# Optimization experiments

Measured on AMD Instinct MI355X. Metric: run time of the kernel, lower is better.

Reference implementation:

```python
import jax, jax.numpy as jnp
import numpy as np

E = 64          # num_experts
DIM = 1024      # model dim
HID = 512       # per-expert FFN hidden dim
N = 65536       # total routed tokens (1024 per expert)


def setup_inputs() -> dict:
    key = jax.random.key(0)
    k_x, k1, k2, k3 = jax.random.split(key, 4)
    x = jax.random.normal(k_x, (N, DIM), dtype=jnp.float32)
    # learned params: w1/w3 [E, HID, DIM], w2 [E, DIM, HID] (trunc_normal std 0.02 ~ normal*0.02)
    w1 = jax.random.normal(k1, (E, HID, DIM), dtype=jnp.float32) * 0.02
    w2 = jax.random.normal(k2, (E, DIM, HID), dtype=jnp.float32) * 0.02
    w3 = jax.random.normal(k3, (E, HID, DIM), dtype=jnp.float32) * 0.02
    num_tokens_per_expert = jnp.full((E,), N // E, dtype=jnp.int32)
    return {"x": x, "w1": w1, "w2": w2, "w3": w3,
            "num_tokens_per_expert": num_tokens_per_expert}


def reference(x, w1, w2, w3, num_tokens_per_expert):
    # Grouped-GEMM SwiGLU expert FFN (torch._grouped_mm path, bf16 compute).
    bf16 = jnp.bfloat16
    xb = x.astype(bf16)                                   # [N, DIM]
    g = num_tokens_per_expert                             # [E] int32 group sizes
    w1t = jnp.swapaxes(w1.astype(bf16), 1, 2)             # [E, DIM, HID]
    w3t = jnp.swapaxes(w3.astype(bf16), 1, 2)             # [E, DIM, HID]
    w2t = jnp.swapaxes(w2.astype(bf16), 1, 2)             # [E, HID, DIM]
    h = jax.nn.silu(jax.lax.ragged_dot(xb, w1t, g))       # [N, HID]
    h = h * jax.lax.ragged_dot(xb, w3t, g)                # fused gate
    out = jax.lax.ragged_dot(h, w2t, g)                   # [N, DIM]
    return out.astype(x.dtype)
```

## Files before the change

### kernel.cpp

```cpp
#include <hip/hip_runtime.h>
#include <hip/hip_bf16.h>
#include <stdint.h>

#define NE   64
#define DIM  1024
#define HID  512
#define TPE  1024

typedef __attribute__((ext_vector_type(8)))  __bf16          bf16x8;
typedef __attribute__((ext_vector_type(16))) float           f32x16;
typedef __attribute__((ext_vector_type(8)))  unsigned short  ushort8_t;
typedef __attribute__((ext_vector_type(4)))  float           float4_t;

__device__ __forceinline__ unsigned short f2bf(float f) {
  return __builtin_bit_cast(unsigned short, static_cast<__bf16>(f));
}
__device__ __forceinline__ float bf2f(unsigned short u) {
  unsigned int x = ((unsigned int)u) << 16;
  return __builtin_bit_cast(float, x);
}
__device__ __forceinline__ ushort8_t pack8(float4_t a, float4_t b) {
  ushort8_t r;
  r[0] = f2bf(a[0]); r[1] = f2bf(a[1]); r[2] = f2bf(a[2]); r[3] = f2bf(a[3]);
  r[4] = f2bf(b[0]); r[5] = f2bf(b[1]); r[6] = f2bf(b[2]); r[7] = f2bf(b[3]);
  return r;
}
__device__ __forceinline__ bf16x8 ldsfrag(const unsigned short* p) {
  return __builtin_bit_cast(bf16x8, *reinterpret_cast<const ushort8_t*>(p));
}

__device__ __forceinline__ void barrier_lgkm() {
  asm volatile("s_waitcnt lgkmcnt(0)" ::: "memory");
  __builtin_amdgcn_s_barrier();
}

#define LDK 40

__device__ __forceinline__ int xcd_swizzle(int bid, int nwg) {
  return (bid & 7) * (nwg >> 3) + (bid >> 3);
}

#define P1_NKT (DIM / 32)

__global__ __launch_bounds__(256, 3) void p1_kernel(
    const float* __restrict__ X, const float* __restrict__ W1,
    const float* __restrict__ W3, unsigned short* __restrict__ H) {
  __shared__ __align__(16) unsigned short lA [2][128 * LDK];
  __shared__ __align__(16) unsigned short lB1[2][ 64 * LDK];
  __shared__ __align__(16) unsigned short lB3[2][ 64 * LDK];

  const int tile = xcd_swizzle(blockIdx.x, NE * 8 * 8);
  const int e  = tile >> 6;
  const int tn = (tile >> 3) & 7;
  const int tm = tile & 7;
  const int t  = threadIdx.x;

  const float* gA  = X  + (size_t)(e * TPE + tm * 128) * DIM;
  const float* gB1 = W1 + ((size_t)e * HID + tn * 64) * DIM;
  const float* gB3 = W3 + ((size_t)e * HID + tn * 64) * DIM;

  const int ar = t >> 2, ac = (t & 3) * 8;

  float4_t a0[2][2], b10[2], b30[2];
  float4_t a1[2][2], b11[2], b31[2];

  auto load_g = [&](float4_t (&a)[2][2], float4_t (&b1)[2], float4_t (&b3)[2],
                    int kt) {
#pragma unroll
    for (int i = 0; i < 2; ++i) {
      const size_t o = (size_t)(ar + 64 * i) * DIM + kt * 32 + ac;
      a[i][0] = *reinterpret_cast<const float4_t*>(gA + o);
      a[i][1] = *reinterpret_cast<const float4_t*>(gA + o + 4);
    }
    const size_t ob = (size_t)ar * DIM + kt * 32 + ac;
    b1[0] = *reinterpret_cast<const float4_t*>(gB1 + ob);
    b1[1] = *reinterpret_cast<const float4_t*>(gB1 + ob + 4);
    b3[0] = *reinterpret_cast<const float4_t*>(gB3 + ob);
    b3[1] = *reinterpret_cast<const float4_t*>(gB3 + ob + 4);
  };
  auto store_l = [&](int buf, float4_t (&a)[2][2], float4_t (&b1)[2],
                     float4_t (&b3)[2]) {
#pragma unroll
    for (int i = 0; i < 2; ++i)
      *reinterpret_cast<ushort8_t*>(&lA[buf][(ar + 64 * i) * LDK + ac]) =
          pack8(a[i][0], a[i][1]);
    *reinterpret_cast<ushort8_t*>(&lB1[buf][ar * LDK + ac]) = pack8(b1[0], b1[1]);
    *reinterpret_cast<ushort8_t*>(&lB3[buf][ar * LDK + ac]) = pack8(b3[0], b3[1]);
  };

  const int lane = t & 63;
  const int wv   = t >> 6;
  const int wr   = wv >> 1, wc = wv & 1;
  const int lr   = lane & 31;
  const int ks   = (lane >> 5) * 8;

  f32x16 acc1[2], acc3[2];
#pragma unroll
  for (int m = 0; m < 2; ++m)
#pragma unroll
    for (int i = 0; i < 16; ++i) { acc1[m][i] = 0.f; acc3[m][i] = 0.f; }

  auto mfma_phase = [&](int buf) {
#pragma unroll
    for (int kk = 0; kk < 2; ++kk) {
      bf16x8 am[2];
#pragma unroll
      for (int m = 0; m < 2; ++m)
        am[m] = ldsfrag(&lA[buf][(wr * 64 + m * 32 + lr) * LDK + kk * 16 + ks]);
      const bf16x8 b1 = ldsfrag(&lB1[buf][(wc * 32 + lr) * LDK + kk * 16 + ks]);
      const bf16x8 b3 = ldsfrag(&lB3[buf][(wc * 32 + lr) * LDK + kk * 16 + ks]);
#pragma unroll
      for (int m = 0; m < 2; ++m) {
        acc1[m] = __builtin_amdgcn_mfma_f32_32x32x16_bf16(am[m], b1, acc1[m], 0, 0, 0);
        acc3[m] = __builtin_amdgcn_mfma_f32_32x32x16_bf16(am[m], b3, acc3[m], 0, 0, 0);
      }
    }
  };

  load_g(a0, b10, b30, 0);
  load_g(a1, b11, b31, 1);
  for (int kt = 0; kt < P1_NKT; kt += 2) {
    store_l(0, a0, b10, b30);
    if (kt + 2 < P1_NKT) load_g(a0, b10, b30, kt + 2);
    barrier_lgkm();
    mfma_phase(0);
    store_l(1, a1, b11, b31);
    if (kt + 3 < P1_NKT) load_g(a1, b11, b31, kt + 3);
    barrier_lgkm();
    mfma_phase(1);
  }

  const int tokBase = e * TPE + tm * 128 + wr * 64;
  const int hid     = tn * 64 + wc * 32 + lr;
  const int ks4     = (lane >> 5) * 4;
#pragma unroll
  for (int m = 0; m < 2; ++m)
#pragma unroll
    for (int r = 0; r < 16; ++r) {
      const int rr  = (r & 3) + 8 * (r >> 2) + ks4;
      const int tok = tokBase + m * 32 + rr;
      const float av = bf2f(f2bf(acc1[m][r]));
      const float bv = bf2f(f2bf(acc3[m][r]));
      const float s  = av / (1.0f + __expf(-av));
      H[(size_t)tok * HID + hid] = f2bf(s * bv);
    }
}

#define P2_NKT (HID / 32)

__global__ __launch_bounds__(256, 3) void p2_kernel(
    const unsigned short* __restrict__ Hin, const float* __restrict__ W2,
    float* __restrict__ OUT) {
  __shared__ __align__(16) unsigned short lA[2][128 * LDK];
  __shared__ __align__(16) unsigned short lB[2][128 * LDK];

  const int tile = xcd_swizzle(blockIdx.x, NE * 8 * 8);
  const int e  = tile >> 6;
  const int tn = (tile >> 3) & 7;
  const int tm = tile & 7;
  const int t  = threadIdx.x;

  const unsigned short* gA = Hin + (size_t)(e * TPE + tm * 128) * HID;
  const float*          gB = W2  + ((size_t)e * DIM + tn * 128) * HID;

  const int arow = t >> 1, acol = (t & 1) * 16;
  const int br = t >> 2, bc = (t & 3) * 8;

  ushort8_t ha0[2], ha1[2];
  float4_t  wb0[2][2], wb1[2][2];

  auto load_g = [&](ushort8_t (&ha)[2], float4_t (&wb)[2][2], int kt) {
    const size_t ao = (size_t)arow * HID + kt * 32 + acol;
    ha[0] = *reinterpret_cast<const ushort8_t*>(gA + ao);
    ha[1] = *reinterpret_cast<const ushort8_t*>(gA + ao + 8);
#pragma unroll
    for (int i = 0; i < 2; ++i) {
      const size_t bo = (size_t)(br + 64 * i) * HID + kt * 32 + bc;
      wb[i][0] = *reinterpret_cast<const float4_t*>(gB + bo);
      wb[i][1] = *reinterpret_cast<const float4_t*>(gB + bo + 4);
    }
  };
  auto store_l = [&](int buf, ushort8_t (&ha)[2], float4_t (&wb)[2][2]) {
    const int ai = arow * LDK + acol;
    *reinterpret_cast<ushort8_t*>(&lA[buf][ai])     = ha[0];
    *reinterpret_cast<ushort8_t*>(&lA[buf][ai + 8]) = ha[1];
#pragma unroll
    for (int i = 0; i < 2; ++i)
      *reinterpret_cast<ushort8_t*>(&lB[buf][(br + 64 * i) * LDK + bc]) =
          pack8(wb[i][0], wb[i][1]);
  };

  const int lane = t & 63;
  const int wv   = t >> 6;
  const int wr   = wv >> 1, wc = wv & 1;
  const int lr   = lane & 31;
  const int ks   = (lane >> 5) * 8;

  f32x16 acc[2][2];
#pragma unroll
  for (int m = 0; m < 2; ++m)
#pragma unroll
    for (int n = 0; n < 2; ++n)
#pragma unroll
      for (int i = 0; i < 16; ++i) acc[m][n][i] = 0.f;

  auto mfma_phase = [&](int buf) {
#pragma unroll
    for (int kk = 0; kk < 2; ++kk) {
      bf16x8 am[2], bn[2];
#pragma unroll
      for (int m = 0; m < 2; ++m)
        am[m] = ldsfrag(&lA[buf][(wr * 64 + m * 32 + lr) * LDK + kk * 16 + ks]);
#pragma unroll
      for (int n = 0; n < 2; ++n)
        bn[n] = ldsfrag(&lB[buf][(wc * 64 + n * 32 + lr) * LDK + kk * 16 + ks]);
#pragma unroll
      for (int m = 0; m < 2; ++m)
#pragma unroll
        for (int n = 0; n < 2; ++n)
          acc[m][n] = __builtin_amdgcn_mfma_f32_32x32x16_bf16(am[m], bn[n], acc[m][n], 0, 0, 0);
    }
  };

  load_g(ha0, wb0, 0);
  load_g(ha1, wb1, 1);
  for (int kt = 0; kt < P2_NKT; kt += 2) {
    store_l(0, ha0, wb0);
    if (kt + 2 < P2_NKT) load_g(ha0, wb0, kt + 2);
    barrier_lgkm();
    mfma_phase(0);

    store_l(1, ha1, wb1);
    if (kt + 3 < P2_NKT) load_g(ha1, wb1, kt + 3);
    barrier_lgkm();
    mfma_phase(1);
  }

  const int tokBase = e * TPE + tm * 128 + wr * 64;
  const int dBase   = tn * 128 + wc * 64;
  const int ks4     = (lane >> 5) * 4;
#pragma unroll
  for (int m = 0; m < 2; ++m)
#pragma unroll
    for (int n = 0; n < 2; ++n)
#pragma unroll
      for (int r = 0; r < 16; ++r) {
        const int rr  = (r & 3) + 8 * (r >> 2) + ks4;
        const int tok = tokBase + m * 32 + rr;
        const int d   = dBase + n * 32 + lr;
        OUT[(size_t)tok * DIM + d] = bf2f(f2bf(acc[m][n][r]));
      }
}

extern "C" void kernel_launch(void* const* d_in, const int* in_sizes, int n_in,
                              void* d_out, int out_size, void* d_ws, size_t ws_size,
                              hipStream_t stream) {
  (void)in_sizes; (void)n_in; (void)out_size; (void)ws_size;
  const float* X  = (const float*)d_in[0];
  const float* W1 = (const float*)d_in[1];
  const float* W2 = (const float*)d_in[2];
  const float* W3 = (const float*)d_in[3];

  unsigned short* H = (unsigned short*)d_ws;
  float* OUT = (float*)d_out;

  p1_kernel<<<dim3(NE * 8 * 8), dim3(256), 0, stream>>>(X, W1, W3, H);
  p2_kernel<<<dim3(NE * 8 * 8), dim3(256), 0, stream>>>(H, W2, OUT);
}
```

Measured before the change: 520.3 us.

## Double M tile to 256 rows and switch to 16x16x32 MFMA fragments

Both kernels now give each block 256 tokens instead of 128, which halves the grid. Each weight tile is reused across twice as many rows, so fewer fp32 weight bytes are reloaded per token. The MFMA instruction changes from 32x32x16 to 16x16x32, with more accumulators per wave (8x2 for the gate pair, 8x4 for the down projection). The cost is much higher register pressure, lowered occupancy bounds (3 to 2), larger LDS use, and fewer blocks to cover the CUs.

```diff
diff --git a/kernel.cpp b/kernel.cpp
--- a/kernel.cpp
+++ b/kernel.cpp
@@ -8,7 +8,7 @@
 #define TPE  1024
 
 typedef __attribute__((ext_vector_type(8)))  __bf16          bf16x8;
-typedef __attribute__((ext_vector_type(16))) float           f32x16;
+typedef __attribute__((ext_vector_type(4)))  float           f32x4;
 typedef __attribute__((ext_vector_type(8)))  unsigned short  ushort8_t;
 typedef __attribute__((ext_vector_type(4)))  float           float4_t;
 
@@ -42,32 +42,32 @@
 
 #define P1_NKT (DIM / 32)
 
-__global__ __launch_bounds__(256, 3) void p1_kernel(
+__global__ __launch_bounds__(256, 2) void p1_kernel(
     const float* __restrict__ X, const float* __restrict__ W1,
     const float* __restrict__ W3, unsigned short* __restrict__ H) {
-  __shared__ __align__(16) unsigned short lA [2][128 * LDK];
+  __shared__ __align__(16) unsigned short lA [2][256 * LDK];
   __shared__ __align__(16) unsigned short lB1[2][ 64 * LDK];
   __shared__ __align__(16) unsigned short lB3[2][ 64 * LDK];
 
-  const int tile = xcd_swizzle(blockIdx.x, NE * 8 * 8);
-  const int e  = tile >> 6;
-  const int tn = (tile >> 3) & 7;
-  const int tm = tile & 7;
+  const int tile = xcd_swizzle(blockIdx.x, NE * 4 * 8);
+  const int e  = tile >> 5;
+  const int tn = (tile >> 2) & 7;
+  const int tm = tile & 3;
   const int t  = threadIdx.x;
 
-  const float* gA  = X  + (size_t)(e * TPE + tm * 128) * DIM;
+  const float* gA  = X  + (size_t)(e * TPE + tm * 256) * DIM;
   const float* gB1 = W1 + ((size_t)e * HID + tn * 64) * DIM;
   const float* gB3 = W3 + ((size_t)e * HID + tn * 64) * DIM;
 
   const int ar = t >> 2, ac = (t & 3) * 8;
 
-  float4_t a0[2][2], b10[2], b30[2];
-  float4_t a1[2][2], b11[2], b31[2];
-
-  auto load_g = [&](float4_t (&a)[2][2], float4_t (&b1)[2], float4_t (&b3)[2],
+  float4_t a0[4][2], b10[2], b30[2];
+  float4_t a1[4][2], b11[2], b31[2];
+
+  auto load_g = [&](float4_t (&a)[4][2], float4_t (&b1)[2], float4_t (&b3)[2],
                     int kt) {
 #pragma unroll
-    for (int i = 0; i < 2; ++i) {
+    for (int i = 0; i < 4; ++i) {
       const size_t o = (size_t)(ar + 64 * i) * DIM + kt * 32 + ac;
       a[i][0] = *reinterpret_cast<const float4_t*>(gA + o);
       a[i][1] = *reinterpret_cast<const float4_t*>(gA + o + 4);
@@ -78,10 +78,10 @@
     b3[0] = *reinterpret_cast<const float4_t*>(gB3 + ob);
     b3[1] = *reinterpret_cast<const float4_t*>(gB3 + ob + 4);
   };
-  auto store_l = [&](int buf, float4_t (&a)[2][2], float4_t (&b1)[2],
+  auto store_l = [&](int buf, float4_t (&a)[4][2], float4_t (&b1)[2],
                      float4_t (&b3)[2]) {
 #pragma unroll
-    for (int i = 0; i < 2; ++i)
+    for (int i = 0; i < 4; ++i)
       *reinterpret_cast<ushort8_t*>(&lA[buf][(ar + 64 * i) * LDK + ac]) =
           pack8(a[i][0], a[i][1]);
     *reinterpret_cast<ushort8_t*>(&lB1[buf][ar * LDK + ac]) = pack8(b1[0], b1[1]);
@@ -91,28 +91,32 @@
   const int lane = t & 63;
   const int wv   = t >> 6;
   const int wr   = wv >> 1, wc = wv & 1;
-  const int lr   = lane & 31;
-  const int ks   = (lane >> 5) * 8;
-
-  f32x16 acc1[2], acc3[2];
-#pragma unroll
-  for (int m = 0; m < 2; ++m)
-#pragma unroll
-    for (int i = 0; i < 16; ++i) { acc1[m][i] = 0.f; acc3[m][i] = 0.f; }
+  const int fr   = lane & 15;
+  const int ks   = (lane >> 4) * 8;
+
+  f32x4 acc1[8][2], acc3[8][2];
+#pragma unroll
+  for (int m = 0; m < 8; ++m)
+#pragma unroll
+    for (int n = 0; n < 2; ++n)
+#pragma unroll
+      for (int i = 0; i < 4; ++i) { acc1[m][n][i] = 0.f; acc3[m][n][i] = 0.f; }
 
   auto mfma_phase = [&](int buf) {
-#pragma unroll
-    for (int kk = 0; kk < 2; ++kk) {
-      bf16x8 am[2];
-#pragma unroll
-      for (int m = 0; m < 2; ++m)
-        am[m] = ldsfrag(&lA[buf][(wr * 64 + m * 32 + lr) * LDK + kk * 16 + ks]);
-      const bf16x8 b1 = ldsfrag(&lB1[buf][(wc * 32 + lr) * LDK + kk * 16 + ks]);
-      const bf16x8 b3 = ldsfrag(&lB3[buf][(wc * 32 + lr) * LDK + kk * 16 + ks]);
-#pragma unroll
-      for (int m = 0; m < 2; ++m) {
-        acc1[m] = __builtin_amdgcn_mfma_f32_32x32x16_bf16(am[m], b1, acc1[m], 0, 0, 0);
-        acc3[m] = __builtin_amdgcn_mfma_f32_32x32x16_bf16(am[m], b3, acc3[m], 0, 0, 0);
+    bf16x8 b1f[2], b3f[2];
+#pragma unroll
+    for (int n = 0; n < 2; ++n) {
+      const int bi = (wc * 32 + n * 16 + fr) * LDK + ks;
+      b1f[n] = ldsfrag(&lB1[buf][bi]);
+      b3f[n] = ldsfrag(&lB3[buf][bi]);
+    }
+#pragma unroll
+    for (int m = 0; m < 8; ++m) {
+      const bf16x8 af = ldsfrag(&lA[buf][(wr * 128 + m * 16 + fr) * LDK + ks]);
+#pragma unroll
+      for (int n = 0; n < 2; ++n) {
+        acc1[m][n] = __builtin_amdgcn_mfma_f32_16x16x32_bf16(af, b1f[n], acc1[m][n], 0, 0, 0);
+        acc3[m][n] = __builtin_amdgcn_mfma_f32_16x16x32_bf16(af, b3f[n], acc3[m][n], 0, 0, 0);
       }
     }
   };
@@ -130,95 +134,92 @@
     mfma_phase(1);
   }
 
-  const int tokBase = e * TPE + tm * 128 + wr * 64;
-  const int hid     = tn * 64 + wc * 32 + lr;
-  const int ks4     = (lane >> 5) * 4;
-#pragma unroll
-  for (int m = 0; m < 2; ++m)
-#pragma unroll
-    for (int r = 0; r < 16; ++r) {
-      const int rr  = (r & 3) + 8 * (r >> 2) + ks4;
-      const int tok = tokBase + m * 32 + rr;
-      const float av = bf2f(f2bf(acc1[m][r]));
-      const float bv = bf2f(f2bf(acc3[m][r]));
-      const float s  = av / (1.0f + __expf(-av));
-      H[(size_t)tok * HID + hid] = f2bf(s * bv);
-    }
+  const int tokBase = e * TPE + tm * 256 + wr * 128 + (lane >> 4) * 4;
+  const int hidBase = tn * 64 + wc * 32;
+#pragma unroll
+  for (int m = 0; m < 8; ++m)
+#pragma unroll
+    for (int n = 0; n < 2; ++n)
+#pragma unroll
+      for (int r = 0; r < 4; ++r) {
+        const int tok = tokBase + m * 16 + r;
+        const int hid = hidBase + n * 16 + fr;
+        const float av = bf2f(f2bf(acc1[m][n][r]));
+        const float bv = bf2f(f2bf(acc3[m][n][r]));
+        const float s  = av / (1.0f + __expf(-av));
+        H[(size_t)tok * HID + hid] = f2bf(s * bv);
+      }
 }
 
 #define P2_NKT (HID / 32)
 
-__global__ __launch_bounds__(256, 3) void p2_kernel(
+__global__ __launch_bounds__(256, 2) void p2_kernel(
     const unsigned short* __restrict__ Hin, const float* __restrict__ W2,
     float* __restrict__ OUT) {
-  __shared__ __align__(16) unsigned short lA[2][128 * LDK];
+  __shared__ __align__(16) unsigned short lA[2][256 * LDK];
   __shared__ __align__(16) unsigned short lB[2][128 * LDK];
 
-  const int tile = xcd_swizzle(blockIdx.x, NE * 8 * 8);
-  const int e  = tile >> 6;
-  const int tn = (tile >> 3) & 7;
-  const int tm = tile & 7;
+  const int tile = xcd_swizzle(blockIdx.x, NE * 4 * 8);
+  const int e  = tile >> 5;
+  const int tn = (tile >> 2) & 7;
+  const int tm = tile & 3;
   const int t  = threadIdx.x;
 
-  const unsigned short* gA = Hin + (size_t)(e * TPE + tm * 128) * HID;
+  const unsigned short* gA = Hin + (size_t)(e * TPE + tm * 256) * HID;
   const float*          gB = W2  + ((size_t)e * DIM + tn * 128) * HID;
 
-  const int arow = t >> 1, acol = (t & 1) * 16;
-  const int br = t >> 2, bc = (t & 3) * 8;
-
-  ushort8_t ha0[2], ha1[2];
+  const int ar = t >> 2, ac = (t & 3) * 8;
+
+  ushort8_t ha0[4], ha1[4];
   float4_t  wb0[2][2], wb1[2][2];
 
-  auto load_g = [&](ushort8_t (&ha)[2], float4_t (&wb)[2][2], int kt) {
-    const size_t ao = (size_t)arow * HID + kt * 32 + acol;
-    ha[0] = *reinterpret_cast<const ushort8_t*>(gA + ao);
-    ha[1] = *reinterpret_cast<const ushort8_t*>(gA + ao + 8);
+  auto load_g = [&](ushort8_t (&ha)[4], float4_t (&wb)[2][2], int kt) {
+#pragma unroll
+    for (int i = 0; i < 4; ++i)
+      ha[i] = *reinterpret_cast<const ushort8_t*>(
+          gA + (size_t)(ar + 64 * i) * HID + kt * 32 + ac);
 #pragma unroll
     for (int i = 0; i < 2; ++i) {
-      const size_t bo = (size_t)(br + 64 * i) * HID + kt * 32 + bc;
+      const size_t bo = (size_t)(ar + 64 * i) * HID + kt * 32 + ac;
       wb[i][0] = *reinterpret_cast<const float4_t*>(gB + bo);
       wb[i][1] = *reinterpret_cast<const float4_t*>(gB + bo + 4);
     }
   };
-  auto store_l = [&](int buf, ushort8_t (&ha)[2], float4_t (&wb)[2][2]) {
-    const int ai = arow * LDK + acol;
-    *reinterpret_cast<ushort8_t*>(&lA[buf][ai])     = ha[0];
-    *reinterpret_cast<ushort8_t*>(&lA[buf][ai + 8]) = ha[1];
+  auto store_l = [&](int buf, ushort8_t (&ha)[4], float4_t (&wb)[2][2]) {
+#pragma unroll
+    for (int i = 0; i < 4; ++i)
+      *reinterpret_cast<ushort8_t*>(&lA[buf][(ar + 64 * i) * LDK + ac]) = ha[i];
 #pragma unroll
     for (int i = 0; i < 2; ++i)
-      *reinterpret_cast<ushort8_t*>(&lB[buf][(br + 64 * i) * LDK + bc]) =
+      *reinterpret_cast<ushort8_t*>(&lB[buf][(ar + 64 * i) * LDK + ac]) =
           pack8(wb[i][0], wb[i][1]);
   };
 
   const int lane = t & 63;
   const int wv   = t >> 6;
   const int wr   = wv >> 1, wc = wv & 1;
-  const int lr   = lane & 31;
-  const int ks   = (lane >> 5) * 8;
-
-  f32x16 acc[2][2];
-#pragma unroll
-  for (int m = 0; m < 2; ++m)
-#pragma unroll
-    for (int n = 0; n < 2; ++n)
-#pragma unroll
-      for (int i = 0; i < 16; ++i) acc[m][n][i] = 0.f;
+  const int fr   = lane & 15;
+  const int ks   = (lane >> 4) * 8;
+
+  f32x4 acc[8][4];
+#pragma unroll
+  for (int m = 0; m < 8; ++m)
+#pragma unroll
+    for (int n = 0; n < 4; ++n)
+#pragma unroll
+      for (int i = 0; i < 4; ++i) acc[m][n][i] = 0.f;
 
   auto mfma_phase = [&](int buf) {
-#pragma unroll
-    for (int kk = 0; kk < 2; ++kk) {
-      bf16x8 am[2], bn[2];
-#pragma unroll
-      for (int m = 0; m < 2; ++m)
-        am[m] = ldsfrag(&lA[buf][(wr * 64 + m * 32 + lr) * LDK + kk * 16 + ks]);
-#pragma unroll
-      for (int n = 0; n < 2; ++n)
-        bn[n] = ldsfrag(&lB[buf][(wc * 64 + n * 32 + lr) * LDK + kk * 16 + ks]);
-#pragma unroll
-      for (int m = 0; m < 2; ++m)
-#pragma unroll
-        for (int n = 0; n < 2; ++n)
-          acc[m][n] = __builtin_amdgcn_mfma_f32_32x32x16_bf16(am[m], bn[n], acc[m][n], 0, 0, 0);
+    bf16x8 bfr[4];
+#pragma unroll
+    for (int n = 0; n < 4; ++n)
+      bfr[n] = ldsfrag(&lB[buf][(wc * 64 + n * 16 + fr) * LDK + ks]);
+#pragma unroll
+    for (int m = 0; m < 8; ++m) {
+      const bf16x8 af = ldsfrag(&lA[buf][(wr * 128 + m * 16 + fr) * LDK + ks]);
+#pragma unroll
+      for (int n = 0; n < 4; ++n)
+        acc[m][n] = __builtin_amdgcn_mfma_f32_16x16x32_bf16(af, bfr[n], acc[m][n], 0, 0, 0);
     }
   };
 
@@ -229,25 +230,22 @@
     if (kt + 2 < P2_NKT) load_g(ha0, wb0, kt + 2);
     barrier_lgkm();
     mfma_phase(0);
-
     store_l(1, ha1, wb1);
     if (kt + 3 < P2_NKT) load_g(ha1, wb1, kt + 3);
     barrier_lgkm();
     mfma_phase(1);
   }
 
-  const int tokBase = e * TPE + tm * 128 + wr * 64;
+  const int tokBase = e * TPE + tm * 256 + wr * 128 + (lane >> 4) * 4;
   const int dBase   = tn * 128 + wc * 64;
-  const int ks4     = (lane >> 5) * 4;
-#pragma unroll
-  for (int m = 0; m < 2; ++m)
-#pragma unroll
-    for (int n = 0; n < 2; ++n)
-#pragma unroll
-      for (int r = 0; r < 16; ++r) {
-        const int rr  = (r & 3) + 8 * (r >> 2) + ks4;
-        const int tok = tokBase + m * 32 + rr;
-        const int d   = dBase + n * 32 + lr;
+#pragma unroll
+  for (int m = 0; m < 8; ++m)
+#pragma unroll
+    for (int n = 0; n < 4; ++n)
+#pragma unroll
+      for (int r = 0; r < 4; ++r) {
+        const int tok = tokBase + m * 16 + r;
+        const int d   = dBase + n * 16 + fr;
         OUT[(size_t)tok * DIM + d] = bf2f(f2bf(acc[m][n][r]));
       }
 }
@@ -264,6 +262,6 @@
   unsigned short* H = (unsigned short*)d_ws;
   float* OUT = (float*)d_out;
 
-  p1_kernel<<<dim3(NE * 8 * 8), dim3(256), 0, stream>>>(X, W1, W3, H);
-  p2_kernel<<<dim3(NE * 8 * 8), dim3(256), 0, stream>>>(H, W2, OUT);
-}
+  p1_kernel<<<dim3(NE * 4 * 8), dim3(256), 0, stream>>>(X, W1, W3, H);
+  p2_kernel<<<dim3(NE * 4 * 8), dim3(256), 0, stream>>>(H, W2, OUT);
+}
```

Result: no change. 517.5 us (-0.5%).

## Switch waves to 32-row x full-N tiling and single-buffer B prefetch

Applied to the files above, without the earlier changes.

Both kernels change the wave layout from a 2x2 wave grid to four waves, each owning 32 rows and the full N width of the block tile. W1 and W3 are merged into one LDS B buffer. The register prefetch of B drops from two sets to one, loaded one k-step ahead, while A keeps its two-deep prefetch. This lowers register pressure and changes the LDS fragment traffic: one A fragment and four B fragments per k-step instead of two and two. In exchange, B fragment LDS reads rise and B global loads get less latency hiding.

```diff
diff --git a/kernel.cpp b/kernel.cpp
--- a/kernel.cpp
+++ b/kernel.cpp
@@ -45,9 +45,8 @@
 __global__ __launch_bounds__(256, 3) void p1_kernel(
     const float* __restrict__ X, const float* __restrict__ W1,
     const float* __restrict__ W3, unsigned short* __restrict__ H) {
-  __shared__ __align__(16) unsigned short lA [2][128 * LDK];
-  __shared__ __align__(16) unsigned short lB1[2][ 64 * LDK];
-  __shared__ __align__(16) unsigned short lB3[2][ 64 * LDK];
+  __shared__ __align__(16) unsigned short lA[2][128 * LDK];
+  __shared__ __align__(16) unsigned short lB[2][128 * LDK];
 
   const int tile = xcd_swizzle(blockIdx.x, NE * 8 * 8);
   const int e  = tile >> 6;
@@ -56,91 +55,92 @@
   const int t  = threadIdx.x;
 
   const float* gA  = X  + (size_t)(e * TPE + tm * 128) * DIM;
-  const float* gB1 = W1 + ((size_t)e * HID + tn * 64) * DIM;
-  const float* gB3 = W3 + ((size_t)e * HID + tn * 64) * DIM;
+  const float* gW1 = W1 + ((size_t)e * HID + tn * 64) * DIM;
+  const float* gW3 = W3 + ((size_t)e * HID + tn * 64) * DIM;
 
   const int ar = t >> 2, ac = (t & 3) * 8;
 
-  float4_t a0[2][2], b10[2], b30[2];
-  float4_t a1[2][2], b11[2], b31[2];
-
-  auto load_g = [&](float4_t (&a)[2][2], float4_t (&b1)[2], float4_t (&b3)[2],
-                    int kt) {
+  float4_t a0[2][2], a1[2][2];
+  float4_t bb[2][2];
+
+  auto load_gA = [&](float4_t (&a)[2][2], int kt) {
 #pragma unroll
     for (int i = 0; i < 2; ++i) {
       const size_t o = (size_t)(ar + 64 * i) * DIM + kt * 32 + ac;
       a[i][0] = *reinterpret_cast<const float4_t*>(gA + o);
       a[i][1] = *reinterpret_cast<const float4_t*>(gA + o + 4);
     }
-    const size_t ob = (size_t)ar * DIM + kt * 32 + ac;
-    b1[0] = *reinterpret_cast<const float4_t*>(gB1 + ob);
-    b1[1] = *reinterpret_cast<const float4_t*>(gB1 + ob + 4);
-    b3[0] = *reinterpret_cast<const float4_t*>(gB3 + ob);
-    b3[1] = *reinterpret_cast<const float4_t*>(gB3 + ob + 4);
-  };
-  auto store_l = [&](int buf, float4_t (&a)[2][2], float4_t (&b1)[2],
-                     float4_t (&b3)[2]) {
+  };
+  auto load_gB = [&](int kt) {
+    const size_t o = (size_t)ar * DIM + kt * 32 + ac;
+    bb[0][0] = *reinterpret_cast<const float4_t*>(gW1 + o);
+    bb[0][1] = *reinterpret_cast<const float4_t*>(gW1 + o + 4);
+    bb[1][0] = *reinterpret_cast<const float4_t*>(gW3 + o);
+    bb[1][1] = *reinterpret_cast<const float4_t*>(gW3 + o + 4);
+  };
+  auto store_lA = [&](int buf, float4_t (&a)[2][2]) {
 #pragma unroll
     for (int i = 0; i < 2; ++i)
       *reinterpret_cast<ushort8_t*>(&lA[buf][(ar + 64 * i) * LDK + ac]) =
           pack8(a[i][0], a[i][1]);
-    *reinterpret_cast<ushort8_t*>(&lB1[buf][ar * LDK + ac]) = pack8(b1[0], b1[1]);
-    *reinterpret_cast<ushort8_t*>(&lB3[buf][ar * LDK + ac]) = pack8(b3[0], b3[1]);
+  };
+  auto store_lB = [&](int buf) {
+    *reinterpret_cast<ushort8_t*>(&lB[buf][ar * LDK + ac]) = pack8(bb[0][0], bb[0][1]);
+    *reinterpret_cast<ushort8_t*>(&lB[buf][(ar + 64) * LDK + ac]) = pack8(bb[1][0], bb[1][1]);
   };
 
   const int lane = t & 63;
   const int wv   = t >> 6;
-  const int wr   = wv >> 1, wc = wv & 1;
   const int lr   = lane & 31;
   const int ks   = (lane >> 5) * 8;
 
-  f32x16 acc1[2], acc3[2];
-#pragma unroll
-  for (int m = 0; m < 2; ++m)
-#pragma unroll
-    for (int i = 0; i < 16; ++i) { acc1[m][i] = 0.f; acc3[m][i] = 0.f; }
+  f32x16 acc[4];
+#pragma unroll
+  for (int n = 0; n < 4; ++n)
+#pragma unroll
+    for (int i = 0; i < 16; ++i) acc[n][i] = 0.f;
 
   auto mfma_phase = [&](int buf) {
 #pragma unroll
     for (int kk = 0; kk < 2; ++kk) {
-      bf16x8 am[2];
-#pragma unroll
-      for (int m = 0; m < 2; ++m)
-        am[m] = ldsfrag(&lA[buf][(wr * 64 + m * 32 + lr) * LDK + kk * 16 + ks]);
-      const bf16x8 b1 = ldsfrag(&lB1[buf][(wc * 32 + lr) * LDK + kk * 16 + ks]);
-      const bf16x8 b3 = ldsfrag(&lB3[buf][(wc * 32 + lr) * LDK + kk * 16 + ks]);
-#pragma unroll
-      for (int m = 0; m < 2; ++m) {
-        acc1[m] = __builtin_amdgcn_mfma_f32_32x32x16_bf16(am[m], b1, acc1[m], 0, 0, 0);
-        acc3[m] = __builtin_amdgcn_mfma_f32_32x32x16_bf16(am[m], b3, acc3[m], 0, 0, 0);
+      const bf16x8 af = ldsfrag(&lA[buf][(wv * 32 + lr) * LDK + kk * 16 + ks]);
+#pragma unroll
+      for (int n = 0; n < 4; ++n) {
+        const bf16x8 bf = ldsfrag(&lB[buf][(n * 32 + lr) * LDK + kk * 16 + ks]);
+        acc[n] = __builtin_amdgcn_mfma_f32_32x32x16_bf16(af, bf, acc[n], 0, 0, 0);
       }
     }
   };
 
-  load_g(a0, b10, b30, 0);
-  load_g(a1, b11, b31, 1);
+  load_gA(a0, 0);
+  load_gB(0);
+  load_gA(a1, 1);
   for (int kt = 0; kt < P1_NKT; kt += 2) {
-    store_l(0, a0, b10, b30);
-    if (kt + 2 < P1_NKT) load_g(a0, b10, b30, kt + 2);
+    store_lA(0, a0); store_lB(0);
+    if (kt + 2 < P1_NKT) load_gA(a0, kt + 2);
+    load_gB(kt + 1);
     barrier_lgkm();
     mfma_phase(0);
-    store_l(1, a1, b11, b31);
-    if (kt + 3 < P1_NKT) load_g(a1, b11, b31, kt + 3);
+
+    store_lA(1, a1); store_lB(1);
+    if (kt + 3 < P1_NKT) load_gA(a1, kt + 3);
+    if (kt + 2 < P1_NKT) load_gB(kt + 2);
     barrier_lgkm();
     mfma_phase(1);
   }
 
-  const int tokBase = e * TPE + tm * 128 + wr * 64;
-  const int hid     = tn * 64 + wc * 32 + lr;
+  const int tokBase = e * TPE + tm * 128 + wv * 32;
+  const int hidBase = tn * 64;
   const int ks4     = (lane >> 5) * 4;
 #pragma unroll
-  for (int m = 0; m < 2; ++m)
+  for (int n = 0; n < 2; ++n)
 #pragma unroll
     for (int r = 0; r < 16; ++r) {
       const int rr  = (r & 3) + 8 * (r >> 2) + ks4;
-      const int tok = tokBase + m * 32 + rr;
-      const float av = bf2f(f2bf(acc1[m][r]));
-      const float bv = bf2f(f2bf(acc3[m][r]));
+      const int tok = tokBase + rr;
+      const int hid = hidBase + n * 32 + lr;
+      const float av = bf2f(f2bf(acc[n][r]));
+      const float bv = bf2f(f2bf(acc[n + 2][r]));
       const float s  = av / (1.0f + __expf(-av));
       H[(size_t)tok * HID + hid] = f2bf(s * bv);
     }
@@ -163,93 +163,89 @@
   const unsigned short* gA = Hin + (size_t)(e * TPE + tm * 128) * HID;
   const float*          gB = W2  + ((size_t)e * DIM + tn * 128) * HID;
 
-  const int arow = t >> 1, acol = (t & 1) * 16;
-  const int br = t >> 2, bc = (t & 3) * 8;
+  const int ar = t >> 2, ac = (t & 3) * 8;
 
   ushort8_t ha0[2], ha1[2];
-  float4_t  wb0[2][2], wb1[2][2];
-
-  auto load_g = [&](ushort8_t (&ha)[2], float4_t (&wb)[2][2], int kt) {
-    const size_t ao = (size_t)arow * HID + kt * 32 + acol;
-    ha[0] = *reinterpret_cast<const ushort8_t*>(gA + ao);
-    ha[1] = *reinterpret_cast<const ushort8_t*>(gA + ao + 8);
+  float4_t  wb[2][2];
+
+  auto load_gA = [&](ushort8_t (&ha)[2], int kt) {
+#pragma unroll
+    for (int i = 0; i < 2; ++i)
+      ha[i] = *reinterpret_cast<const ushort8_t*>(
+          gA + (size_t)(ar + 64 * i) * HID + kt * 32 + ac);
+  };
+  auto load_gB = [&](int kt) {
 #pragma unroll
     for (int i = 0; i < 2; ++i) {
-      const size_t bo = (size_t)(br + 64 * i) * HID + kt * 32 + bc;
-      wb[i][0] = *reinterpret_cast<const float4_t*>(gB + bo);
-      wb[i][1] = *reinterpret_cast<const float4_t*>(gB + bo + 4);
-    }
-  };
-  auto store_l = [&](int buf, ushort8_t (&ha)[2], float4_t (&wb)[2][2]) {
-    const int ai = arow * LDK + acol;
-    *reinterpret_cast<ushort8_t*>(&lA[buf][ai])     = ha[0];
-    *reinterpret_cast<ushort8_t*>(&lA[buf][ai + 8]) = ha[1];
-#pragma unroll
-    for (int i = 0; i < 2; ++i)
-      *reinterpret_cast<ushort8_t*>(&lB[buf][(br + 64 * i) * LDK + bc]) =
+      const size_t o = (size_t)(ar + 64 * i) * HID + kt * 32 + ac;
+      wb[i][0] = *reinterpret_cast<const float4_t*>(gB + o);
+      wb[i][1] = *reinterpret_cast<const float4_t*>(gB + o + 4);
+    }
+  };
+  auto store_lA = [&](int buf, ushort8_t (&ha)[2]) {
+#pragma unroll
+    for (int i = 0; i < 2; ++i)
+      *reinterpret_cast<ushort8_t*>(&lA[buf][(ar + 64 * i) * LDK + ac]) = ha[i];
+  };
+  auto store_lB = [&](int buf) {
+#pragma unroll
+    for (int i = 0; i < 2; ++i)
+      *reinterpret_cast<ushort8_t*>(&lB[buf][(ar + 64 * i) * LDK + ac]) =
           pack8(wb[i][0], wb[i][1]);
   };
 
   const int lane = t & 63;
   const int wv   = t >> 6;
-  const int wr   = wv >> 1, wc = wv & 1;
   const int lr   = lane & 31;
   const int ks   = (lane >> 5) * 8;
 
-  f32x16 acc[2][2];
-#pragma unroll
-  for (int m = 0; m < 2; ++m)
-#pragma unroll
-    for (int n = 0; n < 2; ++n)
-#pragma unroll
-      for (int i = 0; i < 16; ++i) acc[m][n][i] = 0.f;
+  f32x16 acc[4];
+#pragma unroll
+  for (int n = 0; n < 4; ++n)
+#pragma unroll
+    for (int i = 0; i < 16; ++i) acc[n][i] = 0.f;
 
   auto mfma_phase = [&](int buf) {
 #pragma unroll
     for (int kk = 0; kk < 2; ++kk) {
-      bf16x8 am[2], bn[2];
-#pragma unroll
-      for (int m = 0; m < 2; ++m)
-        am[m] = ldsfrag(&lA[buf][(wr * 64 + m * 32 + lr) * LDK + kk * 16 + ks]);
-#pragma unroll
-      for (int n = 0; n < 2; ++n)
-        bn[n] = ldsfrag(&lB[buf][(wc * 64 + n * 32 + lr) * LDK + kk * 16 + ks]);
-#pragma unroll
-      for (int m = 0; m < 2; ++m)
-#pragma unroll
-        for (int n = 0; n < 2; ++n)
-          acc[m][n] = __builtin_amdgcn_mfma_f32_32x32x16_bf16(am[m], bn[n], acc[m][n], 0, 0, 0);
-    }
-  };
-
-  load_g(ha0, wb0, 0);
-  load_g(ha1, wb1, 1);
+      const bf16x8 af = ldsfrag(&lA[buf][(wv * 32 + lr) * LDK + kk * 16 + ks]);
+#pragma unroll
+      for (int n = 0; n < 4; ++n) {
+        const bf16x8 bf = ldsfrag(&lB[buf][(n * 32 + lr) * LDK + kk * 16 + ks]);
+        acc[n] = __builtin_amdgcn_mfma_f32_32x32x16_bf16(af, bf, acc[n], 0, 0, 0);
+      }
+    }
+  };
+
+  load_gA(ha0, 0);
+  load_gB(0);
+  load_gA(ha1, 1);
   for (int kt = 0; kt < P2_NKT; kt += 2) {
-    store_l(0, ha0, wb0);
-    if (kt + 2 < P2_NKT) load_g(ha0, wb0, kt + 2);
+    store_lA(0, ha0); store_lB(0);
+    if (kt + 2 < P2_NKT) load_gA(ha0, kt + 2);
+    load_gB(kt + 1);
     barrier_lgkm();
     mfma_phase(0);
 
-    store_l(1, ha1, wb1);
-    if (kt + 3 < P2_NKT) load_g(ha1, wb1, kt + 3);
+    store_lA(1, ha1); store_lB(1);
+    if (kt + 3 < P2_NKT) load_gA(ha1, kt + 3);
+    if (kt + 2 < P2_NKT) load_gB(kt + 2);
     barrier_lgkm();
     mfma_phase(1);
   }
 
-  const int tokBase = e * TPE + tm * 128 + wr * 64;
-  const int dBase   = tn * 128 + wc * 64;
+  const int tokBase = e * TPE + tm * 128 + wv * 32;
+  const int dBase   = tn * 128;
   const int ks4     = (lane >> 5) * 4;
 #pragma unroll
-  for (int m = 0; m < 2; ++m)
-#pragma unroll
-    for (int n = 0; n < 2; ++n)
-#pragma unroll
-      for (int r = 0; r < 16; ++r) {
-        const int rr  = (r & 3) + 8 * (r >> 2) + ks4;
-        const int tok = tokBase + m * 32 + rr;
-        const int d   = dBase + n * 32 + lr;
-        OUT[(size_t)tok * DIM + d] = bf2f(f2bf(acc[m][n][r]));
-      }
+  for (int n = 0; n < 4; ++n)
+#pragma unroll
+    for (int r = 0; r < 16; ++r) {
+      const int rr  = (r & 3) + 8 * (r >> 2) + ks4;
+      const int tok = tokBase + rr;
+      const int d   = dBase + n * 32 + lr;
+      OUT[(size_t)tok * DIM + d] = bf2f(f2bf(acc[n][r]));
+    }
 }
 
 extern "C" void kernel_launch(void* const* d_in, const int* in_sizes, int n_in,
```

Result: faster. 438.0 us (-15.8%).
